# Performance work log

Measured on AMD Instinct MI355X. Metric: run time of the kernel, lower is better.

## Reference

```python
import jax, jax.numpy as jnp
import numpy as np

N, D = 4096, 128  # seq length / feature dim of x is N; head dim is D

def setup_inputs() -> dict:
    key = jax.random.key(0)
    k1, k2 = jax.random.split(key)
    x = jax.random.normal(k1, (N, N), dtype=jnp.float32)
    # nn.Linear(N, 3*d): weight [3d, N], bias [3d]; scale weight like torch init
    W = jax.random.normal(k2, (3 * D, N), dtype=jnp.float32) / jnp.sqrt(jnp.float32(N))
    b = jnp.zeros((3 * D,), dtype=jnp.float32)
    return {"x": x, "W": W, "b": b}

def reference(x, W, b):
    # QKV projection: [N, 3d]
    qkv = x @ W.T + b
    Q, K, V = jnp.split(qkv, 3, axis=-1)  # each [N, d]
    # The blockwise online-softmax double loop computes exactly
    # softmax(Q K^T) V with NO 1/sqrt(d) scaling (faithful to source).
    S = Q @ K.T                 # [N, N]
    P = jax.nn.softmax(S, axis=-1)
    return P @ V                # [N, d]
```

## Files before the change

kernel.cpp:

```cpp
#include <hip/hip_runtime.h>
#include <cstdint>
#include <cstddef>

typedef _Float16 f16;
typedef f16 f16x8 __attribute__((ext_vector_type(8)));
typedef f16 f16x4 __attribute__((ext_vector_type(4)));
typedef float f32x4 __attribute__((ext_vector_type(4)));

#define SEQ 4096
#define DH 128
#define QKV_LD 384
#define LOG2E 1.44269504f

__device__ __forceinline__ float fast_exp2(float x) {
#if __has_builtin(__builtin_amdgcn_exp2f)
  return __builtin_amdgcn_exp2f(x);
#else
  return exp2f(x);
#endif
}

__global__ __launch_bounds__(256) void cvt_w_kernel(const float4* __restrict__ W,
                                                    f16x4* __restrict__ Wh) {
  int i = blockIdx.x * 256 + threadIdx.x;
  float4 v = W[i];
  f16x4 h; h[0] = (f16)v.x; h[1] = (f16)v.y; h[2] = (f16)v.z; h[3] = (f16)v.w;
  Wh[i] = h;
}

template <int SPLITS>
__global__ __launch_bounds__(256) void gemm_qkv(const float* __restrict__ x,
                                                const f16* __restrict__ Wh,
                                                f16* __restrict__ part) {
  __shared__ f16 Ax[128][72];
  __shared__ f16 Bx[128][72];
  const int m0 = blockIdx.x * 128;
  const int n0 = blockIdx.y * 128;
  const int split = blockIdx.z;
  const int k0 = split * (SEQ / SPLITS);
  const int tid = threadIdx.x;
  const int lane = tid & 63, wave = tid >> 6;
  const int wr = (wave >> 1) * 64, wc = (wave & 1) * 64;
  const int l15 = lane & 15, quad = lane >> 4;

  f32x4 acc[4][4] = {};

  for (int kt = k0; kt < k0 + SEQ / SPLITS; kt += 64) {
#pragma unroll
    for (int r = 0; r < 8; ++r) {
      int c = tid + r * 256;
      int row = c >> 4, col = (c & 15) * 4;
      float4 v = *(const float4*)&x[(size_t)(m0 + row) * SEQ + kt + col];
      f16x4 h; h[0] = (f16)v.x; h[1] = (f16)v.y; h[2] = (f16)v.z; h[3] = (f16)v.w;
      *(f16x4*)&Ax[row][col] = h;
    }
#pragma unroll
    for (int r = 0; r < 4; ++r) {
      int c = tid + r * 256;
      int row = c >> 3, col = (c & 7) * 8;
      *(f16x8*)&Bx[row][col] = *(const f16x8*)&Wh[(size_t)(n0 + row) * SEQ + kt + col];
    }
    __syncthreads();
#pragma unroll
    for (int ks = 0; ks < 2; ++ks) {
      f16x8 a[4], bb[4];
#pragma unroll
      for (int t = 0; t < 4; ++t) {
        a[t]  = *(const f16x8*)&Ax[wr + t * 16 + l15][ks * 32 + quad * 8];
        bb[t] = *(const f16x8*)&Bx[wc + t * 16 + l15][ks * 32 + quad * 8];
      }
#pragma unroll
      for (int mt = 0; mt < 4; ++mt)
#pragma unroll
        for (int nt = 0; nt < 4; ++nt)
          acc[mt][nt] = __builtin_amdgcn_mfma_f32_16x16x32_f16(a[mt], bb[nt], acc[mt][nt], 0, 0, 0);
    }
    __syncthreads();
  }

  f16* pw = part + (size_t)split * SEQ * QKV_LD;
#pragma unroll
  for (int mt = 0; mt < 4; ++mt) {
#pragma unroll
    for (int nt = 0; nt < 4; ++nt) {
      int col = n0 + wc + nt * 16 + l15;
      int rowbase = m0 + wr + mt * 16 + quad * 4;
#pragma unroll
      for (int rr = 0; rr < 4; ++rr)
        pw[(size_t)(rowbase + rr) * QKV_LD + col] = (f16)acc[mt][nt][rr];
    }
  }
}

template <int SPLITS>
__global__ __launch_bounds__(256) void reduce_qkv(const f16* __restrict__ part,
                                                  const float* __restrict__ bias,
                                                  f16* __restrict__ qkv) {
  int i = (blockIdx.x * 256 + threadIdx.x) * 8;
  float acc[8] = {};
#pragma unroll
  for (int s = 0; s < SPLITS; ++s) {
    f16x8 p = *(const f16x8*)&part[(size_t)s * SEQ * QKV_LD + i];
#pragma unroll
    for (int j = 0; j < 8; ++j) acc[j] += (float)p[j];
  }
  int col = i % QKV_LD;
  f16x8 o;
#pragma unroll
  for (int j = 0; j < 8; ++j) o[j] = (f16)(acc[j] + bias[col + j]);
  *(f16x8*)&qkv[i] = o;
}

__global__ __launch_bounds__(256) void transpose_v(const f16* __restrict__ qkv,
                                                   f16* __restrict__ Vt) {
  __shared__ f16 T[64][72];
  const int r0 = blockIdx.x * 64;
  const int c0 = blockIdx.y * 64;
  const int tid = threadIdx.x;
#pragma unroll
  for (int rep = 0; rep < 2; ++rep) {
    int idx = rep * 256 + tid;
    int row = idx >> 3, col = (idx & 7) * 8;
    *(f16x8*)&T[row][col] = *(const f16x8*)&qkv[(size_t)(r0 + row) * QKV_LD + 256 + c0 + col];
  }
  __syncthreads();
#pragma unroll
  for (int rep = 0; rep < 2; ++rep) {
    int idx = rep * 256 + tid;
    int cc = idx >> 3, rb = (idx & 7) * 8;
    f16x8 o;
#pragma unroll
    for (int j = 0; j < 8; ++j) o[j] = T[rb + j][cc];
    *(f16x8*)&Vt[(size_t)(c0 + cc) * SEQ + r0 + rb] = o;
  }
}

#define NSPLIT 16
#define KVRANGE (SEQ / NSPLIT)

__global__ __launch_bounds__(256, 2) void attn_partial(const f16* __restrict__ qkv,
                                                       const f16* __restrict__ Vt,
                                                       f16* __restrict__ Op,
                                                       float* __restrict__ ml) {
  __shared__ f16 Ks[64][136];
  __shared__ f16 Vs[128][72];
  __shared__ f16 Ps[4][32][72];

  const int q0 = blockIdx.x * 128;
  const int split = blockIdx.y;
  const int kv0 = split * KVRANGE;
  const int tid = threadIdx.x;
  const int lane = tid & 63, wave = tid >> 6;
  const int l15 = lane & 15, quad = lane >> 4;
  const int mbase = q0 + wave * 32;

  f16x8 qf[2][4];
#pragma unroll
  for (int mt = 0; mt < 2; ++mt)
#pragma unroll
    for (int ks = 0; ks < 4; ++ks) {
      f16x8 q = *(const f16x8*)&qkv[(size_t)(mbase + mt * 16 + l15) * QKV_LD + ks * 32 + quad * 8];
      qf[mt][ks] = q * (f16)LOG2E;
    }

  f32x4 oacc[2][8] = {};
  float mrow[2][4], lrow[2][4];
#pragma unroll
  for (int mt = 0; mt < 2; ++mt)
#pragma unroll
    for (int rr = 0; rr < 4; ++rr) { mrow[mt][rr] = -1e30f; lrow[mt][rr] = 0.f; }

  for (int it = 0; it < KVRANGE / 64; ++it) {
    const int k0 = kv0 + it * 64;
#pragma unroll
    for (int r = 0; r < 4; ++r) {
      int c = tid + r * 256;
      int row = c >> 4, col = (c & 15) * 8;
      *(f16x8*)&Ks[row][col] = *(const f16x8*)&qkv[(size_t)(k0 + row) * QKV_LD + DH + col];
    }
#pragma unroll
    for (int r = 0; r < 4; ++r) {
      int c = tid + r * 256;
      int row = c >> 3, col = (c & 7) * 8;
      *(f16x8*)&Vs[row][col] = *(const f16x8*)&Vt[(size_t)row * SEQ + k0 + col];
    }
    __syncthreads();

    f32x4 s[2][4] = {};
#pragma unroll
    for (int ks = 0; ks < 4; ++ks) {
      f16x8 kf[4];
#pragma unroll
      for (int nt = 0; nt < 4; ++nt)
        kf[nt] = *(const f16x8*)&Ks[nt * 16 + l15][ks * 32 + quad * 8];
#pragma unroll
      for (int mt = 0; mt < 2; ++mt)
#pragma unroll
        for (int nt = 0; nt < 4; ++nt)
          s[mt][nt] = __builtin_amdgcn_mfma_f32_16x16x32_f16(qf[mt][ks], kf[nt], s[mt][nt], 0, 0, 0);
    }

#pragma unroll
    for (int mt = 0; mt < 2; ++mt) {
      float mnew[4], al[4];
#pragma unroll
      for (int rr = 0; rr < 4; ++rr) {
        float v = s[mt][0][rr];
#pragma unroll
        for (int nt = 1; nt < 4; ++nt) v = fmaxf(v, s[mt][nt][rr]);
        for (int off = 1; off < 16; off <<= 1) v = fmaxf(v, __shfl_xor(v, off));
        mnew[rr] = fmaxf(mrow[mt][rr], v);
        al[rr] = fast_exp2(mrow[mt][rr] - mnew[rr]);
        mrow[mt][rr] = mnew[rr];
      }
      float ls[4] = {0.f, 0.f, 0.f, 0.f};
#pragma unroll
      for (int nt = 0; nt < 4; ++nt)
#pragma unroll
        for (int rr = 0; rr < 4; ++rr) {
          float p = fast_exp2(s[mt][nt][rr] - mnew[rr]);
          ls[rr] += p;
          Ps[wave][mt * 16 + quad * 4 + rr][nt * 16 + l15] = (f16)p;
        }
#pragma unroll
      for (int rr = 0; rr < 4; ++rr) {
        float t = ls[rr];
        for (int off = 1; off < 16; off <<= 1) t += __shfl_xor(t, off);
        lrow[mt][rr] = lrow[mt][rr] * al[rr] + t;
      }
#pragma unroll
      for (int dt = 0; dt < 8; ++dt)
#pragma unroll
        for (int rr = 0; rr < 4; ++rr)
          oacc[mt][dt][rr] *= al[rr];
    }

#pragma unroll
    for (int kk = 0; kk < 2; ++kk) {
      f16x8 pf0 = *(const f16x8*)&Ps[wave][0 + l15][kk * 32 + quad * 8];
      f16x8 pf1 = *(const f16x8*)&Ps[wave][16 + l15][kk * 32 + quad * 8];
#pragma unroll
      for (int dt = 0; dt < 8; ++dt) {
        f16x8 vf = *(const f16x8*)&Vs[dt * 16 + l15][kk * 32 + quad * 8];
        oacc[0][dt] = __builtin_amdgcn_mfma_f32_16x16x32_f16(pf0, vf, oacc[0][dt], 0, 0, 0);
        oacc[1][dt] = __builtin_amdgcn_mfma_f32_16x16x32_f16(pf1, vf, oacc[1][dt], 0, 0, 0);
      }
    }
    __syncthreads();
  }

#pragma unroll
  for (int mt = 0; mt < 2; ++mt) {
#pragma unroll
    for (int dt = 0; dt < 8; ++dt)
#pragma unroll
      for (int rr = 0; rr < 4; ++rr) {
        int row = mbase + mt * 16 + quad * 4 + rr;
        Op[((size_t)split * SEQ + row) * DH + dt * 16 + l15] = (f16)oacc[mt][dt][rr];
      }
    if (l15 == 0) {
#pragma unroll
      for (int rr = 0; rr < 4; ++rr) {
        int row = mbase + mt * 16 + quad * 4 + rr;
        ml[((size_t)split * SEQ + row) * 2 + 0] = mrow[mt][rr];
        ml[((size_t)split * SEQ + row) * 2 + 1] = lrow[mt][rr];
      }
    }
  }
}

__global__ __launch_bounds__(256) void combine_kernel(const f16* __restrict__ Op,
                                                      const float* __restrict__ ml,
                                                      float* __restrict__ out) {
  int idx = blockIdx.x * 256 + threadIdx.x;
  int row = idx >> 7;
  float ms[NSPLIT], ls[NSPLIT];
  float M = -1e30f;
#pragma unroll
  for (int s = 0; s < NSPLIT; ++s) {
    ms[s] = ml[((size_t)s * SEQ + row) * 2 + 0];
    ls[s] = ml[((size_t)s * SEQ + row) * 2 + 1];
    M = fmaxf(M, ms[s]);
  }
  float L = 0.f, o = 0.f;
#pragma unroll
  for (int s = 0; s < NSPLIT; ++s) {
    float w = fast_exp2(ms[s] - M);
    L += ls[s] * w;
    o += w * (float)Op[(size_t)s * SEQ * DH + idx];
  }
  out[idx] = o / L;
}

extern "C" void kernel_launch(void* const* d_in, const int* in_sizes, int n_in,
                              void* d_out, int out_size, void* d_ws, size_t ws_size,
                              hipStream_t stream) {
  const float* x = (const float*)d_in[0];
  const float* W = (const float*)d_in[1];
  const float* b = (const float*)d_in[2];
  float* out = (float*)d_out;
  char* ws = (char*)d_ws;

  f16*   Wh   = (f16*)(ws);
  f16*   qkv  = (f16*)(ws + (3u << 20));
  f16*   Vt   = (f16*)(ws + (6u << 20));
  float* ml   = (float*)(ws + (7u << 20));
  char*  scr  = ws + (7u << 20) + (1u << 19);
  f16*   part = (f16*)scr;
  f16*   Op   = (f16*)scr;

  cvt_w_kernel<<<(384 * 4096 / 4) / 256, 256, 0, stream>>>((const float4*)W, (f16x4*)Wh);

  bool big = ws_size >= ((size_t)32u << 20);
  if (big) {
    gemm_qkv<8><<<dim3(SEQ / 128, 3, 8), 256, 0, stream>>>(x, Wh, part);
    reduce_qkv<8><<<SEQ * QKV_LD / 8 / 256, 256, 0, stream>>>(part, b, qkv);
  } else {
    gemm_qkv<4><<<dim3(SEQ / 128, 3, 4), 256, 0, stream>>>(x, Wh, part);
    reduce_qkv<4><<<SEQ * QKV_LD / 8 / 256, 256, 0, stream>>>(part, b, qkv);
  }
  transpose_v<<<dim3(SEQ / 64, DH / 64), 256, 0, stream>>>(qkv, Vt);
  attn_partial<<<dim3(SEQ / 128, NSPLIT), 256, 0, stream>>>(qkv, Vt, Op, ml);
  combine_kernel<<<(SEQ * DH) / 256, 256, 0, stream>>>(Op, ml, out);
}
```

Before: 165.7 us.

## Retile QKV GEMM to full-width 64x384 blocks and use DPP row reductions in attention

The QKV projection GEMM now gives each block 64 rows and all 384 output columns, so x is read and converted to fp16 once instead of three times, and the kernel requests two blocks per CU. The attention kernel replaces shuffle-based 16-lane max and sum reductions with DPP moves, and stores P transposed as packed f16x4 writes read back with scalar gathers, with an added block barrier. The workspace threshold for choosing 8 splits is lowered slightly. The costs are more LDS for the GEMM B tile, scalar LDS gathers for P fragments, and an extra barrier in the attention loop.

```diff
diff --git a/kernel.cpp b/kernel.cpp
--- a/kernel.cpp
+++ b/kernel.cpp
@@ -20,6 +20,26 @@
 #endif
 }
 
+template <int CTRL>
+__device__ __forceinline__ float dppf(float x) {
+  int r = __builtin_amdgcn_mov_dpp(__builtin_bit_cast(int, x), CTRL, 0xF, 0xF, true);
+  return __builtin_bit_cast(float, r);
+}
+__device__ __forceinline__ float rmax16(float v) {
+  v = fmaxf(v, dppf<0x128>(v));
+  v = fmaxf(v, dppf<0x124>(v));
+  v = fmaxf(v, dppf<0x4E>(v));
+  v = fmaxf(v, dppf<0xB1>(v));
+  return v;
+}
+__device__ __forceinline__ float rsum16(float v) {
+  v += dppf<0x128>(v);
+  v += dppf<0x124>(v);
+  v += dppf<0x4E>(v);
+  v += dppf<0xB1>(v);
+  return v;
+}
+
 __global__ __launch_bounds__(256) void cvt_w_kernel(const float4* __restrict__ W,
                                                     f16x4* __restrict__ Wh) {
   int i = blockIdx.x * 256 + threadIdx.x;
@@ -29,25 +49,24 @@
 }
 
 template <int SPLITS>
-__global__ __launch_bounds__(256) void gemm_qkv(const float* __restrict__ x,
-                                                const f16* __restrict__ Wh,
-                                                f16* __restrict__ part) {
-  __shared__ f16 Ax[128][72];
-  __shared__ f16 Bx[128][72];
-  const int m0 = blockIdx.x * 128;
-  const int n0 = blockIdx.y * 128;
-  const int split = blockIdx.z;
+__global__ __launch_bounds__(256, 2) void gemm_qkv(const float* __restrict__ x,
+                                                   const f16* __restrict__ Wh,
+                                                   f16* __restrict__ part) {
+  __shared__ f16 Ax[64][72];
+  __shared__ f16 Bx[384][72];
+  const int m0 = blockIdx.x * 64;
+  const int split = blockIdx.y;
   const int k0 = split * (SEQ / SPLITS);
   const int tid = threadIdx.x;
   const int lane = tid & 63, wave = tid >> 6;
-  const int wr = (wave >> 1) * 64, wc = (wave & 1) * 64;
+  const int nb = wave * 96;
   const int l15 = lane & 15, quad = lane >> 4;
 
-  f32x4 acc[4][4] = {};
+  f32x4 acc[4][6] = {};
 
   for (int kt = k0; kt < k0 + SEQ / SPLITS; kt += 64) {
 #pragma unroll
-    for (int r = 0; r < 8; ++r) {
+    for (int r = 0; r < 4; ++r) {
       int c = tid + r * 256;
       int row = c >> 4, col = (c & 15) * 4;
       float4 v = *(const float4*)&x[(size_t)(m0 + row) * SEQ + kt + col];
@@ -55,24 +74,25 @@
       *(f16x4*)&Ax[row][col] = h;
     }
 #pragma unroll
-    for (int r = 0; r < 4; ++r) {
+    for (int r = 0; r < 12; ++r) {
       int c = tid + r * 256;
       int row = c >> 3, col = (c & 7) * 8;
-      *(f16x8*)&Bx[row][col] = *(const f16x8*)&Wh[(size_t)(n0 + row) * SEQ + kt + col];
+      *(f16x8*)&Bx[row][col] = *(const f16x8*)&Wh[(size_t)row * SEQ + kt + col];
     }
     __syncthreads();
 #pragma unroll
     for (int ks = 0; ks < 2; ++ks) {
-      f16x8 a[4], bb[4];
-#pragma unroll
-      for (int t = 0; t < 4; ++t) {
-        a[t]  = *(const f16x8*)&Ax[wr + t * 16 + l15][ks * 32 + quad * 8];
-        bb[t] = *(const f16x8*)&Bx[wc + t * 16 + l15][ks * 32 + quad * 8];
-      }
+      f16x8 a[4], bb[6];
+#pragma unroll
+      for (int t = 0; t < 4; ++t)
+        a[t] = *(const f16x8*)&Ax[t * 16 + l15][ks * 32 + quad * 8];
+#pragma unroll
+      for (int t = 0; t < 6; ++t)
+        bb[t] = *(const f16x8*)&Bx[nb + t * 16 + l15][ks * 32 + quad * 8];
 #pragma unroll
       for (int mt = 0; mt < 4; ++mt)
 #pragma unroll
-        for (int nt = 0; nt < 4; ++nt)
+        for (int nt = 0; nt < 6; ++nt)
           acc[mt][nt] = __builtin_amdgcn_mfma_f32_16x16x32_f16(a[mt], bb[nt], acc[mt][nt], 0, 0, 0);
     }
     __syncthreads();
@@ -82,9 +102,9 @@
 #pragma unroll
   for (int mt = 0; mt < 4; ++mt) {
 #pragma unroll
-    for (int nt = 0; nt < 4; ++nt) {
-      int col = n0 + wc + nt * 16 + l15;
-      int rowbase = m0 + wr + mt * 16 + quad * 4;
+    for (int nt = 0; nt < 6; ++nt) {
+      int col = nb + nt * 16 + l15;
+      int rowbase = m0 + mt * 16 + quad * 4;
 #pragma unroll
       for (int rr = 0; rr < 4; ++rr)
         pw[(size_t)(rowbase + rr) * QKV_LD + col] = (f16)acc[mt][nt][rr];
@@ -144,7 +164,7 @@
                                                        float* __restrict__ ml) {
   __shared__ f16 Ks[64][136];
   __shared__ f16 Vs[128][72];
-  __shared__ f16 Ps[4][32][72];
+  __shared__ f16 Pt[4][64][36];
 
   const int q0 = blockIdx.x * 128;
   const int split = blockIdx.y;
@@ -205,45 +225,48 @@
       float mnew[4], al[4];
 #pragma unroll
       for (int rr = 0; rr < 4; ++rr) {
-        float v = s[mt][0][rr];
-#pragma unroll
-        for (int nt = 1; nt < 4; ++nt) v = fmaxf(v, s[mt][nt][rr]);
-        for (int off = 1; off < 16; off <<= 1) v = fmaxf(v, __shfl_xor(v, off));
+        float v = fmaxf(fmaxf(s[mt][0][rr], s[mt][1][rr]), fmaxf(s[mt][2][rr], s[mt][3][rr]));
+        v = rmax16(v);
         mnew[rr] = fmaxf(mrow[mt][rr], v);
         al[rr] = fast_exp2(mrow[mt][rr] - mnew[rr]);
         mrow[mt][rr] = mnew[rr];
       }
       float ls[4] = {0.f, 0.f, 0.f, 0.f};
 #pragma unroll
-      for (int nt = 0; nt < 4; ++nt)
+      for (int nt = 0; nt < 4; ++nt) {
+        f16x4 pk;
 #pragma unroll
         for (int rr = 0; rr < 4; ++rr) {
           float p = fast_exp2(s[mt][nt][rr] - mnew[rr]);
           ls[rr] += p;
-          Ps[wave][mt * 16 + quad * 4 + rr][nt * 16 + l15] = (f16)p;
+          pk[rr] = (f16)p;
         }
-#pragma unroll
-      for (int rr = 0; rr < 4; ++rr) {
-        float t = ls[rr];
-        for (int off = 1; off < 16; off <<= 1) t += __shfl_xor(t, off);
-        lrow[mt][rr] = lrow[mt][rr] * al[rr] + t;
-      }
+        *(f16x4*)&Pt[wave][nt * 16 + l15][mt * 16 + quad * 4] = pk;
+      }
+#pragma unroll
+      for (int rr = 0; rr < 4; ++rr)
+        lrow[mt][rr] = lrow[mt][rr] * al[rr] + rsum16(ls[rr]);
 #pragma unroll
       for (int dt = 0; dt < 8; ++dt)
 #pragma unroll
         for (int rr = 0; rr < 4; ++rr)
           oacc[mt][dt][rr] *= al[rr];
     }
+    __syncthreads();
 
 #pragma unroll
     for (int kk = 0; kk < 2; ++kk) {
-      f16x8 pf0 = *(const f16x8*)&Ps[wave][0 + l15][kk * 32 + quad * 8];
-      f16x8 pf1 = *(const f16x8*)&Ps[wave][16 + l15][kk * 32 + quad * 8];
+      f16x8 pf[2];
+#pragma unroll
+      for (int mt = 0; mt < 2; ++mt)
+#pragma unroll
+        for (int j = 0; j < 8; ++j)
+          pf[mt][j] = Pt[wave][kk * 32 + quad * 8 + j][mt * 16 + l15];
 #pragma unroll
       for (int dt = 0; dt < 8; ++dt) {
         f16x8 vf = *(const f16x8*)&Vs[dt * 16 + l15][kk * 32 + quad * 8];
-        oacc[0][dt] = __builtin_amdgcn_mfma_f32_16x16x32_f16(pf0, vf, oacc[0][dt], 0, 0, 0);
-        oacc[1][dt] = __builtin_amdgcn_mfma_f32_16x16x32_f16(pf1, vf, oacc[1][dt], 0, 0, 0);
+        oacc[0][dt] = __builtin_amdgcn_mfma_f32_16x16x32_f16(pf[0], vf, oacc[0][dt], 0, 0, 0);
+        oacc[1][dt] = __builtin_amdgcn_mfma_f32_16x16x32_f16(pf[1], vf, oacc[1][dt], 0, 0, 0);
       }
     }
     __syncthreads();
@@ -311,12 +334,12 @@
 
   cvt_w_kernel<<<(384 * 4096 / 4) / 256, 256, 0, stream>>>((const float4*)W, (f16x4*)Wh);
 
-  bool big = ws_size >= ((size_t)32u << 20);
+  bool big = ws_size >= ((size_t)31u << 20) + ((size_t)1u << 19);
   if (big) {
-    gemm_qkv<8><<<dim3(SEQ / 128, 3, 8), 256, 0, stream>>>(x, Wh, part);
+    gemm_qkv<8><<<dim3(SEQ / 64, 8), 256, 0, stream>>>(x, Wh, part);
     reduce_qkv<8><<<SEQ * QKV_LD / 8 / 256, 256, 0, stream>>>(part, b, qkv);
   } else {
-    gemm_qkv<4><<<dim3(SEQ / 128, 3, 4), 256, 0, stream>>>(x, Wh, part);
+    gemm_qkv<4><<<dim3(SEQ / 64, 4), 256, 0, stream>>>(x, Wh, part);
     reduce_qkv<4><<<SEQ * QKV_LD / 8 / 256, 256, 0, stream>>>(part, b, qkv);
   }
   transpose_v<<<dim3(SEQ / 64, DH / 64), 256, 0, stream>>>(qkv, Vt);
```

Result: faster. 154.5 us (-6.7%).
